# Kernel optimization log

Hardware: AMD Instinct MI355X
Metric: run time of the kernel (lower is better)

Reference implementation:

```python
import jax, jax.numpy as jnp
import numpy as np

B, F, E = 8192, 64, 32

def setup_inputs() -> dict:
    key = jax.random.key(0)
    x = jax.random.normal(key, (B, F, E), dtype=jnp.float32)
    return {"x": x}

def reference(x) -> jnp.ndarray:
    # Original: elementwise outer product (B,F,F,E), strict-upper-tri mask,
    # flatten row-major to (B, F(F-1)/2, E), then sum over E.
    # Equivalent math: pairwise inner products x_i . x_j for i < j.
    f = x.shape[1]
    gram = jnp.einsum('bie,bje->bij', x, x)  # (B, F, F)
    iu, ju = jnp.triu_indices(f, k=1)        # row-major (i<j), matches boolean_mask order
    return gram[:, iu, ju]                   # (B, F*(F-1)//2)
```

## Files before the change

kernel.cpp:

```cpp
#include <hip/hip_runtime.h>


#define FDIM 64
#define EDIM 32
#define PAIRS 2016

typedef __attribute__((ext_vector_type(8))) short bf16x8;
typedef __attribute__((ext_vector_type(4))) float f32x4;

static __device__ __forceinline__ short f2bf(float f) {
    union { float f; unsigned u; } v; v.f = f;
    unsigned r = v.u + 0x7FFFu + ((v.u >> 16) & 1u);
    return (short)(r >> 16);
}

__global__ __launch_bounds__(256, 8) void ipn_mfma_kernel(const float* __restrict__ x,
                                                          float* __restrict__ out) {
    __shared__ float pbuf[4][1024];

    const int tid = threadIdx.x;
    const int w   = tid >> 6;
    const int l   = tid & 63;
    const int b   = blockIdx.x * 4 + w;

    const int r16 = l & 15;
    const int kb  = (l >> 4) * 8;

    const float* xb = x + (size_t)b * (FDIM * EDIM);

    bf16x8 frag[4];
    #pragma unroll
    for (int p = 0; p < 4; ++p) {
        const float* rp = xb + (p * 16 + r16) * EDIM + kb;
        f32x4 lo = *(const f32x4*)(rp);
        f32x4 hi = *(const f32x4*)(rp + 4);
        bf16x8 f;
        f[0] = f2bf(lo.x); f[1] = f2bf(lo.y); f[2] = f2bf(lo.z); f[3] = f2bf(lo.w);
        f[4] = f2bf(hi.x); f[5] = f2bf(hi.y); f[6] = f2bf(hi.z); f[7] = f2bf(hi.w);
        frag[p] = f;
    }

    f32x4 acc[10];
    #pragma unroll
    for (int t = 0; t < 10; ++t) acc[t] = (f32x4)(0.0f);
    {
        int idx = 0;
        #pragma unroll
        for (int p = 0; p < 4; ++p)
            #pragma unroll
            for (int q = p; q < 4; ++q) {
                acc[idx] = __builtin_amdgcn_mfma_f32_16x16x32_bf16(
                    frag[p], frag[q], acc[idx], 0, 0, 0);
                ++idx;
            }
    }

    float* pb = pbuf[w];
    float* ob = out + (size_t)b * PAIRS;
    const int jc = r16;
    const int ir = (l >> 4) * 4;

    const int base_p[4] = {0, 888, 1520, 1896};
    const int n4_p[4]   = {222, 158, 94, 30};

    {
        int idx = 0;
        #pragma unroll
        for (int p = 0; p < 4; ++p) {
            #pragma unroll
            for (int q = p; q < 4; ++q) {
                const int jg = q * 16 + jc;
                #pragma unroll
                for (int t = 0; t < 4; ++t) {
                    const int ig = p * 16 + ir + t;
                    if (p < q || jg > ig) {
                        const int pos = ig * (2 * FDIM - 1 - ig) / 2 - ig - 1
                                        + jg - base_p[p];
                        pb[pos] = acc[idx][t];
                    }
                }
                ++idx;
            }
            const f32x4* pb4 = (const f32x4*)pb;
            f32x4* ob4 = (f32x4*)(ob + base_p[p]);
            #pragma unroll
            for (int it = 0; it * 64 < n4_p[p]; ++it) {
                const int idx4 = it * 64 + l;
                if (idx4 < n4_p[p]) {
                    f32x4 v = pb4[idx4];
                    __builtin_nontemporal_store(v, ob4 + idx4);
                }
            }
        }
    }
}

extern "C" void kernel_launch(void* const* d_in, const int* in_sizes, int n_in,
                              void* d_out, int out_size, void* d_ws, size_t ws_size,
                              hipStream_t stream) {
    const float* x = (const float*)d_in[0];
    float* out = (float*)d_out;
    const int nb = in_sizes[0] / (FDIM * EDIM);
    const int grid = nb / 4;
    ipn_mfma_kernel<<<grid, 256, 0, stream>>>(x, out);
}
```

Measured before the change: 25.62 us.

## Process two batches per wave, prefetching the second while computing the first

Each wave now handles two batch elements. The raw loads for the second batch are issued before the MFMA and store epilogue of the first, and a sched_barrier keeps the compiler from reordering them, so the second batch's memory latency is hidden behind the first batch's work. The grid is halved, launch bounds drop from 8 to 4 blocks per CU, and the manual bf16 rounding is replaced with the HIP intrinsic. The cost is higher register pressure and fewer resident waves, which may reduce latency hiding from occupancy.

```diff
diff --git a/kernel.cpp b/kernel.cpp
--- a/kernel.cpp
+++ b/kernel.cpp
@@ -1,4 +1,5 @@
 #include <hip/hip_runtime.h>
+#include <hip/hip_bf16.h>
 
 
 #define FDIM 64
@@ -9,37 +10,36 @@
 typedef __attribute__((ext_vector_type(4))) float f32x4;
 
 static __device__ __forceinline__ short f2bf(float f) {
-    union { float f; unsigned u; } v; v.f = f;
-    unsigned r = v.u + 0x7FFFu + ((v.u >> 16) & 1u);
-    return (short)(r >> 16);
+    __hip_bfloat16 h = __float2bfloat16(f);
+    union { __hip_bfloat16 h; short s; } u; u.h = h;
+    return u.s;
 }
 
-__global__ __launch_bounds__(256, 8) void ipn_mfma_kernel(const float* __restrict__ x,
-                                                          float* __restrict__ out) {
-    __shared__ float pbuf[4][1024];
+static __device__ __forceinline__ void cvt_frags(const f32x4 raw[8], bf16x8 frag[4]) {
+    #pragma unroll
+    for (int p = 0; p < 4; ++p) {
+        bf16x8 f;
+        f[0] = f2bf(raw[2*p].x); f[1] = f2bf(raw[2*p].y);
+        f[2] = f2bf(raw[2*p].z); f[3] = f2bf(raw[2*p].w);
+        f[4] = f2bf(raw[2*p+1].x); f[5] = f2bf(raw[2*p+1].y);
+        f[6] = f2bf(raw[2*p+1].z); f[7] = f2bf(raw[2*p+1].w);
+        frag[p] = f;
+    }
+}
 
-    const int tid = threadIdx.x;
-    const int w   = tid >> 6;
-    const int l   = tid & 63;
-    const int b   = blockIdx.x * 4 + w;
-
-    const int r16 = l & 15;
-    const int kb  = (l >> 4) * 8;
-
-    const float* xb = x + (size_t)b * (FDIM * EDIM);
-
-    bf16x8 frag[4];
+static __device__ __forceinline__ void load_raw(const float* __restrict__ xb,
+                                                int r16, int kb, f32x4 raw[8]) {
     #pragma unroll
     for (int p = 0; p < 4; ++p) {
         const float* rp = xb + (p * 16 + r16) * EDIM + kb;
-        f32x4 lo = *(const f32x4*)(rp);
-        f32x4 hi = *(const f32x4*)(rp + 4);
-        bf16x8 f;
-        f[0] = f2bf(lo.x); f[1] = f2bf(lo.y); f[2] = f2bf(lo.z); f[3] = f2bf(lo.w);
-        f[4] = f2bf(hi.x); f[5] = f2bf(hi.y); f[6] = f2bf(hi.z); f[7] = f2bf(hi.w);
-        frag[p] = f;
+        raw[2*p]   = *(const f32x4*)(rp);
+        raw[2*p+1] = *(const f32x4*)(rp + 4);
     }
+}
 
+static __device__ __forceinline__ void epilogue(const bf16x8 frag[4],
+                                                float* __restrict__ pb,
+                                                float* __restrict__ ob, int l) {
     f32x4 acc[10];
     #pragma unroll
     for (int t = 0; t < 10; ++t) acc[t] = (f32x4)(0.0f);
@@ -55,14 +55,10 @@
             }
     }
 
-    float* pb = pbuf[w];
-    float* ob = out + (size_t)b * PAIRS;
-    const int jc = r16;
+    const int jc = l & 15;
     const int ir = (l >> 4) * 4;
-
     const int base_p[4] = {0, 888, 1520, 1896};
     const int n4_p[4]   = {222, 158, 94, 30};
-
     {
         int idx = 0;
         #pragma unroll
@@ -95,12 +91,44 @@
     }
 }
 
+__global__ __launch_bounds__(256, 4) void ipn_mfma_kernel(const float* __restrict__ x,
+                                                          float* __restrict__ out) {
+    __shared__ float pbuf[4][1024];
+
+    const int tid = threadIdx.x;
+    const int w   = tid >> 6;
+    const int l   = tid & 63;
+    const int wid = blockIdx.x * 4 + w;
+    const int b0  = wid * 2;
+    const int b1  = b0 + 1;
+
+    const int r16 = l & 15;
+    const int kb  = (l >> 4) * 8;
+
+    float* pb = pbuf[w];
+
+    f32x4 raw0[8];
+    load_raw(x + (size_t)b0 * (FDIM * EDIM), r16, kb, raw0);
+    bf16x8 frag0[4];
+    cvt_frags(raw0, frag0);
+
+    f32x4 raw1[8];
+    load_raw(x + (size_t)b1 * (FDIM * EDIM), r16, kb, raw1);
+    __builtin_amdgcn_sched_barrier(0);
+
+    epilogue(frag0, pb, out + (size_t)b0 * PAIRS, l);
+
+    bf16x8 frag1[4];
+    cvt_frags(raw1, frag1);
+    epilogue(frag1, pb, out + (size_t)b1 * PAIRS, l);
+}
+
 extern "C" void kernel_launch(void* const* d_in, const int* in_sizes, int n_in,
                               void* d_out, int out_size, void* d_ws, size_t ws_size,
                               hipStream_t stream) {
     const float* x = (const float*)d_in[0];
     float* out = (float*)d_out;
     const int nb = in_sizes[0] / (FDIM * EDIM);
-    const int grid = nb / 4;
+    const int grid = nb / 8;
     ipn_mfma_kernel<<<grid, 256, 0, stream>>>(x, out);
 }
```

Measured after the change: 25.83 us. About the same (+0.8%).
